# Optimization experiments

Measured on AMD Instinct MI355X. Metric: run time of the kernel, lower is better.

Reference implementation:

```python
import jax, jax.numpy as jnp
import numpy as np
import math

MAX_L = 2          # max spherical-harmonic order
C = 16             # channels per l (num_channels)
LAYERS = 2         # num_CG_layers
CUT = 0.5          # hard_cut_rad


def _cg_single(j1, m1, j2, m2, j, m):
    # Racah formula for Clebsch-Gordan coefficient <j1 m1 j2 m2 | j m>
    if m1 + m2 != m:
        return 0.0
    f = math.factorial
    pre = math.sqrt((2 * j + 1) * f(j + j1 - j2) * f(j - j1 + j2) * f(j1 + j2 - j) / f(j1 + j2 + j + 1))
    pre *= math.sqrt(f(j + m) * f(j - m) * f(j1 - m1) * f(j1 + m1) * f(j2 - m2) * f(j2 + m2))
    s = 0.0
    for k in range(max(0, j2 - j - m1, j1 + m2 - j), min(j1 + j2 - j, j1 - m1, j2 + m2) + 1):
        s += (-1) ** k / (f(k) * f(j1 + j2 - j - k) * f(j1 - m1 - k) * f(j2 + m2 - k) * f(j - j2 + m1 + k) * f(j - j1 - m2 + k))
    return pre * s


PAIRS = {l: [(l1, l2) for l1 in range(MAX_L + 1) for l2 in range(MAX_L + 1) if abs(l1 - l2) <= l <= l1 + l2]
         for l in range(MAX_L + 1)}
CG = {}
for _l in range(MAX_L + 1):
    for (_l1, _l2) in PAIRS[_l]:
        t = np.zeros((2 * _l1 + 1, 2 * _l2 + 1, 2 * _l + 1), np.float32)
        for i1 in range(2 * _l1 + 1):
            for i2 in range(2 * _l2 + 1):
                m = (i1 - _l1) + (i2 - _l2)
                if -_l <= m <= _l:
                    t[i1, i2, m + _l] = _cg_single(_l1, i1 - _l1, _l2, i2 - _l2, _l, m)
        CG[(_l1, _l2, _l)] = jnp.asarray(t)


def _sph(rel_pos):
    # real spherical harmonics Y_l^m of relative positions, l=0..2; [B,N,N,2l+1]
    r = jnp.sqrt(jnp.sum(rel_pos ** 2, -1)) + 1e-6
    x = rel_pos[..., 0] / r
    y = rel_pos[..., 1] / r
    z = rel_pos[..., 2] / r
    Y0 = jnp.full(r.shape + (1,), 0.28209479, rel_pos.dtype)
    Y1 = 0.48860251 * jnp.stack([y, z, x], -1)
    Y2 = jnp.stack([1.09254843 * x * y, 1.09254843 * y * z, 0.31539157 * (3.0 * z * z - 1.0),
                    1.09254843 * x * z, 0.54627422 * (x * x - y * y)], -1)
    return [Y0, Y1, Y2]


def _cgprod(A, B, diag):
    # CG tensor product; full product concatenates outer-product channels (c,d),
    # Diag product pairs channels diagonally (c with c).
    out = []
    for l in range(MAX_L + 1):
        segs = []
        for (l1, l2) in PAIRS[l]:
            cg = CG[(l1, l2, l)]
            if diag:
                segs.append(jnp.einsum('bnmc,bnuc,muk->bnkc', A[l1], B[l2], cg))
            else:
                s = jnp.einsum('bnmc,bnud,muk->bnkcd', A[l1], B[l2], cg)
                segs.append(s.reshape(s.shape[:3] + (-1,)))
        out.append(jnp.concatenate(segs, -1))
    return out


def _normalize(parts):
    # NormalizeVecArr: divide part_l by (2l+1)*||part_l||_F / num_channels
    return [p * (C / ((2 * l + 1) * jnp.linalg.norm(p))) for l, p in enumerate(parts)]


def reference(v0, v1, v2, rel_pos, norms, Wr0, Wr1, Wr2, Wn0, Wn1, Wn2):
    verts = [v0, v1, v2]
    Y = _sph(rel_pos)
    # sphx: sum sph over neighbor axis j (einsum 'bijmc->bimc'), broadcast to C channels
    sphx = []
    for y in Y:
        s = y.sum(2)  # [B,N,2l+1]
        sphx.append(jnp.broadcast_to(s[..., None], s.shape + (C,)))
    conn = (norms < CUT).astype(rel_pos.dtype)  # [B,N,N] connectivity mask
    Wr = [Wr0, Wr1, Wr2]
    Wn = [Wn0, Wn1, Wn2]
    scal = []
    for layer in range(LAYERS):
        cg_rel = _cgprod(verts, sphx, diag=False)
        rel_mixed = [jnp.einsum('bnkp,pc->bnkc', cg_rel[l], Wr[l][layer]) for l in range(MAX_L + 1)]
        # message pass: masked gather-sum over neighbors
        mp = [jnp.einsum('bij,bjkc->bikc', conn, rel_mixed[l]) for l in range(MAX_L + 1)]
        cg_nl = _cgprod(mp, mp, diag=True)
        nl_mixed = [jnp.einsum('bnkp,pc->bnkc', cg_nl[l], Wn[l][layer]) for l in range(MAX_L + 1)]
        verts = _normalize(nl_mixed)
        # GetScalars: l=0 part plus per-l SO(3)-invariant norms sum_m v^2
        s0 = verts[0][:, :, 0, :]                                   # [B,N,C]
        sn = [jnp.sum(verts[l] * verts[l], axis=2) for l in range(MAX_L + 1)]
        scal.append(jnp.concatenate([s0] + sn, -1))                 # [B,N,4C]
    return jnp.concatenate(scal, -1)  # [B,N,LAYERS*4*C]


def setup_inputs():
    B, N = 32, 128
    ks = jax.random.split(jax.random.key(0), 11)
    return {
        'v0': jax.random.normal(ks[0], (B, N, 1, C), jnp.float32),
        'v1': jax.random.normal(ks[1], (B, N, 3, C), jnp.float32),
        'v2': jax.random.normal(ks[2], (B, N, 5, C), jnp.float32),
        'rel_pos': jax.random.normal(ks[3], (B, N, N, 3), jnp.float32),
        'norms': jax.random.uniform(ks[4], (B, N, N), jnp.float32),
        'Wr0': jax.random.normal(ks[5], (LAYERS, 3 * C * C, C), jnp.float32),
        'Wr1': jax.random.normal(ks[6], (LAYERS, 6 * C * C, C), jnp.float32),
        'Wr2': jax.random.normal(ks[7], (LAYERS, 6 * C * C, C), jnp.float32),
        'Wn0': jax.random.normal(ks[8], (LAYERS, 3 * C, C), jnp.float32),
        'Wn1': jax.random.normal(ks[9], (LAYERS, 6 * C, C), jnp.float32),
        'Wn2': jax.random.normal(ks[10], (LAYERS, 6 * C, C), jnp.float32),
    }
```

## Files before the change

kernel.cpp:

```cpp
#include <hip/hip_runtime.h>

#define NN 128

__constant__ int E_l [15] = {0,0,0, 1,1,1,1,1,1, 2,2,2,2,2,2};
__constant__ int E_l1[15] = {0,1,2, 0,1,1,1,2,2, 0,1,1,2,2,2};
__constant__ int E_l2[15] = {0,1,2, 1,0,1,2,1,2, 2,1,2,0,1,2};
__constant__ int E_cg[15] = {0,1,10, 35,44,53,80,125,170, 245,270,315,390,415,490};
__constant__ int E_t [15] = {0,16,32, 48,96,144,192,240,288, 336,416,496,576,656,736};

__device__ __forceinline__ double dfact(int n){
    const double F[9] = {1.0,1.0,2.0,6.0,24.0,120.0,720.0,5040.0,40320.0};
    return F[n];
}

__device__ float cg_single(int j1,int m1,int j2,int m2,int j,int m){
    if (m1 + m2 != m) return 0.0f;
    double pre = sqrt((2.0*j+1.0)*dfact(j+j1-j2)*dfact(j-j1+j2)*dfact(j1+j2-j)/dfact(j1+j2+j+1));
    pre *= sqrt(dfact(j+m)*dfact(j-m)*dfact(j1-m1)*dfact(j1+m1)*dfact(j2-m2)*dfact(j2+m2));
    int k0 = 0;
    if (j2-j-m1 > k0) k0 = j2-j-m1;
    if (j1+m2-j > k0) k0 = j1+m2-j;
    int k1 = j1+j2-j;
    if (j1-m1 < k1) k1 = j1-m1;
    if (j2+m2 < k1) k1 = j2+m2;
    double s = 0.0;
    for (int k = k0; k <= k1; ++k){
        double d = dfact(k)*dfact(j1+j2-j-k)*dfact(j1-m1-k)*dfact(j2+m2-k)*dfact(j-j2+m1+k)*dfact(j-j1-m2+k);
        s += ((k & 1) ? -1.0 : 1.0) / d;
    }
    return (float)(pre * s);
}


__global__ __launch_bounds__(512) void k_setup(const float* __restrict__ Wr0, const float* __restrict__ Wr1,
                                               const float* __restrict__ Wr2,
                                               float* __restrict__ blob, float* __restrict__ wrsum){
    int bx = blockIdx.x, t = threadIdx.x;
    if (bx == 0){
        for (int idx = t; idx < 615; idx += 512){
            int e = 0;
            while (e < 14 && idx >= E_cg[e+1]) e++;
            int l = E_l[e], l1 = E_l1[e], l2 = E_l2[e];
            int local = idx - E_cg[e];
            int dl = 2*l+1, d2 = 2*l2+1;
            int k  = local % dl;
            int r  = local / dl;
            int u  = r % d2;
            int i1 = r / d2;
            blob[idx] = cg_single(l1, i1-l1, l2, u-l2, l, k-l);
        }
        if (t == 0){
            unsigned short* bTB = (unsigned short*)((char*)blob + 2464);
            unsigned char*  bTA = (unsigned char*)((char*)blob + 4096);
            unsigned short* bTC = (unsigned short*)((char*)blob + 4256);
            const int abase[3] = {0,1,4};
            int nt = 0;
            for (int e = 0; e < 15; ++e){
                int l = E_l[e], l1 = E_l1[e], l2 = E_l2[e];
                int dl = 2*l+1, d2 = 2*l2+1;
                for (int k = 0; k < dl; ++k){
                    int st = nt;
                    for (int m = 0; m < 2*l1+1; ++m){
                        int u = k - l + l1 + l2 - m;
                        if (u >= 0 && u <= 2*l2){
                            bTA[nt] = (unsigned char)(((abase[l1]+m)<<4) | (abase[l2]+u));
                            bTC[nt] = (unsigned short)(E_cg[e] + (m*d2+u)*dl + k);
                            nt++;
                        }
                    }
                    int ct = nt - st;
                    for (int c = 0; c < 16; ++c)
                        bTB[E_t[e] + k*16 + c] = (unsigned short)(c | (st<<4) | (ct<<12));
                }
            }
        }
        return;
    }
    int q = (bx-1)*512 + t;
    int layer = q / 3840;
    int r = q % 3840;
    int row = r >> 4, co = r & 15;
    const float* Wr; int pairs; int lrow;
    if (row < 48)       { Wr = Wr0; pairs = 3; lrow = row; }
    else if (row < 144) { Wr = Wr1; pairs = 6; lrow = row - 48; }
    else                { Wr = Wr2; pairs = 6; lrow = row - 144; }
    int pairIdx = lrow >> 4, c = lrow & 15;
    const float* base = Wr + (size_t)layer*pairs*4096 + (size_t)(pairIdx*256 + c*16)*16 + co;
    float s = 0.f;
    #pragma unroll
    for (int d = 0; d < 16; ++d) s += base[d*16];
    wrsum[q] = s;
}

__device__ __forceinline__ void ld_tables(const float* __restrict__ blob, float* CG, unsigned short* TB,
                                          unsigned char* TA, unsigned short* TC, int t){
    for (int i = t; i < 615; i += 512) CG[i] = blob[i];
    const unsigned short* bTB = (const unsigned short*)((const char*)blob + 2464);
    for (int i = t; i < 816; i += 512) TB[i] = bTB[i];
    const unsigned char* bTA = (const unsigned char*)((const char*)blob + 4096);
    if (t < 160) TA[t] = bTA[t];
    const unsigned short* bTC = (const unsigned short*)((const char*)blob + 4256);
    if (t < 160) TC[t] = bTC[t];
}

__device__ __forceinline__ void tfill_full(const float* __restrict__ A, const float* __restrict__ S,
                                           const float* __restrict__ CG, const unsigned short* __restrict__ TB,
                                           const unsigned char* __restrict__ TA, const unsigned short* __restrict__ TC,
                                           float* __restrict__ Tw, int lane){
    #pragma unroll 1
    for (int idx = lane; idx < 816; idx += 64){
        unsigned tbv = TB[idx];
        int c = tbv & 15, st = (tbv>>4) & 255, ct = tbv >> 12;
        float s = 0.f;
        for (int q = 0; q < ct; ++q){
            int ab = TA[st+q];
            s += A[(ab>>4)*16 + c] * S[ab & 15] * CG[TC[st+q]];
        }
        Tw[idx] = s;
    }
}

__device__ __forceinline__ void tfill_diag(const float* __restrict__ M,
                                           const float* __restrict__ CG, const unsigned short* __restrict__ TB,
                                           const unsigned char* __restrict__ TA, const unsigned short* __restrict__ TC,
                                           float* __restrict__ Tw, int lane){
    #pragma unroll 1
    for (int idx = lane; idx < 816; idx += 64){
        unsigned tbv = TB[idx];
        int c = tbv & 15, st = (tbv>>4) & 255, ct = tbv >> 12;
        float s = 0.f;
        for (int q = 0; q < ct; ++q){
            int ab = TA[st+q];
            s += M[(ab>>4)*16 + c] * M[(ab&15)*16 + c] * CG[TC[st+q]];
        }
        Tw[idx] = s;
    }
}

__device__ __forceinline__ float mix_out(const float* __restrict__ WT, const float* __restrict__ Tw, int o){
    int krow = o >> 4, co = o & 15;
    int l = krow == 0 ? 0 : (krow < 4 ? 1 : 2);
    int k = krow - (l==0?0:(l==1?1:4));
    int np = l==0?3:6;
    int tb = l==0?0:(l==1?48:336);
    int rb = l==0?0:(l==1?48:144);
    int dl = 2*l+1;
    float acc = 0.f;
    const float4* Wp = (const float4*)&WT[co*244 + rb];
    #pragma unroll 1
    for (int pq = 0; pq < np; ++pq){
        const float4* Tp = (const float4*)&Tw[tb + (pq*dl + k)*16];
        float4 a0=Tp[0],a1=Tp[1],a2=Tp[2],a3=Tp[3];
        float4 b0=Wp[pq*4],b1=Wp[pq*4+1],b2=Wp[pq*4+2],b3=Wp[pq*4+3];
        acc += a0.x*b0.x+a0.y*b0.y+a0.z*b0.z+a0.w*b0.w
             + a1.x*b1.x+a1.y*b1.y+a1.z*b1.z+a1.w*b1.w
             + a2.x*b2.x+a2.y*b2.y+a2.z*b2.z+a2.w*b2.w
             + a3.x*b3.x+a3.y*b3.y+a3.z*b3.z+a3.w*b3.w;
    }
    return acc;
}

__global__ __launch_bounds__(512) void k_rel0(const float* __restrict__ v0, const float* __restrict__ v1,
                                              const float* __restrict__ v2, const float* __restrict__ rel_pos,
                                              const float* __restrict__ blob, const float* __restrict__ wrsumL,
                                              float* __restrict__ sphx_ws, float* __restrict__ rel){
    __shared__ float CG[616];
    __shared__ unsigned short TB[816];
    __shared__ unsigned char TA[160];
    __shared__ unsigned short TC[160];
    __shared__ float WT[16*244];
    __shared__ float AL[8][144];
    __shared__ float SX[8][12];
    __shared__ __align__(16) float TS[8][816];
    int t = threadIdx.x, w = t >> 6, lane = t & 63;
    int node0 = blockIdx.x * 8, node = node0 + w;
    ld_tables(blob, CG, TB, TA, TC, t);
    #pragma unroll 1
    for (int i = t; i < 3840; i += 512) WT[(i&15)*244 + (i>>4)] = wrsumL[i];
    #pragma unroll 1
    for (int i = t; i < 1152; i += 512){
        int n = i/144, o = i%144, nd = node0+n;
        float v;
        if (o < 16)      v = v0[(size_t)nd*16 + o];
        else if (o < 64) v = v1[(size_t)nd*48 + (o-16)];
        else             v = v2[(size_t)nd*80 + (o-64)];
        AL[n][o] = v;
    }
    {
        const float* rp = rel_pos + (size_t)node * (NN*3);
        float a[9];
        #pragma unroll
        for (int i = 0; i < 9; ++i) a[i] = 0.f;
        #pragma unroll
        for (int rr = 0; rr < 2; ++rr){
            int j = lane + rr*64;
            float x = rp[j*3], y = rp[j*3+1], z = rp[j*3+2];
            float rn = sqrtf(x*x+y*y+z*z) + 1e-6f;
            x /= rn; y /= rn; z /= rn;
            a[0] += 0.28209479f;
            a[1] += 0.48860251f*y; a[2] += 0.48860251f*z; a[3] += 0.48860251f*x;
            a[4] += 1.09254843f*x*y; a[5] += 1.09254843f*y*z;
            a[6] += 0.31539157f*(3.f*z*z-1.f);
            a[7] += 1.09254843f*x*z; a[8] += 0.54627422f*(x*x-y*y);
        }
        #pragma unroll
        for (int i = 0; i < 9; ++i){
            float vv = a[i];
            for (int off = 32; off; off >>= 1) vv += __shfl_down(vv, off, 64);
            if (lane == 0){ SX[w][i] = vv; sphx_ws[(size_t)node*9 + i] = vv; }
        }
    }
    __syncthreads();
    tfill_full(&AL[w][0], &SX[w][0], CG, TB, TA, TC, &TS[w][0], lane);
    __syncthreads();
    float* relw = rel + (size_t)node * 144;
    #pragma unroll 1
    for (int o = lane; o < 144; o += 64) relw[o] = mix_out(WT, &TS[w][0], o);
}

__global__ __launch_bounds__(512) void k_mp(const float* __restrict__ norms, const float* __restrict__ rel,
                                            const float* __restrict__ blob,
                                            const float* __restrict__ Wn0, const float* __restrict__ Wn1,
                                            const float* __restrict__ Wn2, int layer,
                                            float* __restrict__ nl, float* __restrict__ part){
    __shared__ float CG[616];
    __shared__ unsigned short TB[816];
    __shared__ unsigned char TA[160];
    __shared__ unsigned short TC[160];
    __shared__ float WT[16*244];
    __shared__ float C4[8][128];
    __shared__ float MP[8][144];
    __shared__ __align__(16) float TS[8][816];
    __shared__ float RED[24];
    int t = threadIdx.x, w = t >> 6, lane = t & 63;
    int node0 = blockIdx.x * 8, node = node0 + w;
    int b = node0 >> 7;
    ld_tables(blob, CG, TB, TA, TC, t);
    #pragma unroll 1
    for (int i = t; i < 768;  i += 512) WT[(i&15)*244 + (i>>4)]        = Wn0[(size_t)layer*768  + i];
    #pragma unroll 1
    for (int i = t; i < 1536; i += 512) WT[(i&15)*244 + 48  + (i>>4)]  = Wn1[(size_t)layer*1536 + i];
    #pragma unroll 1
    for (int i = t; i < 1536; i += 512) WT[(i&15)*244 + 144 + (i>>4)]  = Wn2[(size_t)layer*1536 + i];
    #pragma unroll 1
    for (int i = t; i < 1024; i += 512){
        int n = i >> 7, j = i & 127;
        C4[n][j] = (norms[(size_t)(node0+n)*NN + j] < 0.5f) ? 1.f : 0.f;
    }
    const float4* r4 = (const float4*)(rel + (size_t)b * NN * 144);
    float4 rA = r4[t];
    float4 rB = r4[512 + t];
    float4 rC = (t < 128) ? r4[1024 + t] : make_float4(0.f,0.f,0.f,0.f);
    float a0 = 0.f, a1 = 0.f, a2 = 0.f;
    float4* s4 = (float4*)&TS[0][0];
    #pragma unroll 1
    for (int r = 0; r < 4; ++r){
        __syncthreads();
        s4[t] = rA; s4[512+t] = rB; if (t < 128) s4[1024+t] = rC;
        __syncthreads();
        if (r < 3){
            rA = r4[(r+1)*1152 + t];
            rB = r4[(r+1)*1152 + 512 + t];
            if (t < 128) rC = r4[(r+1)*1152 + 1024 + t];
        }
        #pragma unroll 4
        for (int jj = 0; jj < 32; ++jj){
            float cn = C4[w][r*32 + jj];
            const float* row = &TS[0][0] + jj*144;
            a0 += cn * row[lane];
            a1 += cn * row[64 + lane];
            if (lane < 16) a2 += cn * row[128 + lane];
        }
    }
    __syncthreads();
    MP[w][lane] = a0; MP[w][64+lane] = a1; if (lane < 16) MP[w][128+lane] = a2;
    __syncthreads();
    tfill_diag(&MP[w][0], CG, TB, TA, TC, &TS[w][0], lane);
    __syncthreads();
    float pz0 = 0.f, pz1 = 0.f, pz2 = 0.f;
    float* nlw = nl + (size_t)node * 144;
    #pragma unroll 1
    for (int o = lane; o < 144; o += 64){
        float acc = mix_out(WT, &TS[w][0], o);
        nlw[o] = acc;
        float sq = acc*acc;
        int krow = o >> 4;
        if (krow == 0) pz0 += sq; else if (krow < 4) pz1 += sq; else pz2 += sq;
    }
    for (int off = 32; off; off >>= 1){
        pz0 += __shfl_down(pz0, off, 64);
        pz1 += __shfl_down(pz1, off, 64);
        pz2 += __shfl_down(pz2, off, 64);
    }
    if (lane == 0){ RED[w] = pz0; RED[8+w] = pz1; RED[16+w] = pz2; }
    __syncthreads();
    if (t < 3){
        float s = 0.f;
        #pragma unroll
        for (int q = 0; q < 8; ++q) s += RED[t*8 + q];
        part[blockIdx.x*4 + t] = s;
    }
}

__global__ __launch_bounds__(512) void k_eb(const float* __restrict__ blob, const float* __restrict__ wrsumL1,
                                            const float* __restrict__ part, const float* __restrict__ nl,
                                            const float* __restrict__ sphx_ws, float* __restrict__ rel,
                                            float* __restrict__ out){
    __shared__ float CG[616];
    __shared__ unsigned short TB[816];
    __shared__ unsigned char TA[160];
    __shared__ unsigned short TC[160];
    __shared__ float WT[16*244];
    __shared__ float AL[8][144];
    __shared__ float SX[8][12];
    __shared__ __align__(16) float TS[8][816];
    __shared__ float RED[24];
    __shared__ float SC[3];
    int t = threadIdx.x, w = t >> 6, lane = t & 63;
    int node0 = blockIdx.x * 8, node = node0 + w;
    ld_tables(blob, CG, TB, TA, TC, t);
    #pragma unroll 1
    for (int i = t; i < 3840; i += 512) WT[(i&15)*244 + (i>>4)] = wrsumL1[i];
    {
        float q0 = part[t*4], q1 = part[t*4+1], q2 = part[t*4+2];
        for (int off = 32; off; off >>= 1){
            q0 += __shfl_down(q0, off, 64);
            q1 += __shfl_down(q1, off, 64);
            q2 += __shfl_down(q2, off, 64);
        }
        if (lane == 0){ RED[w] = q0; RED[8+w] = q1; RED[16+w] = q2; }
    }
    __syncthreads();
    if (t < 3){
        float s = 0.f;
        #pragma unroll
        for (int q = 0; q < 8; ++q) s += RED[t*8 + q];
        SC[t] = 16.f / ((2*t+1) * sqrtf(s));
    }
    __syncthreads();
    float sc0 = SC[0], sc1 = SC[1], sc2 = SC[2];
    #pragma unroll 1
    for (int i = t; i < 1152; i += 512){
        int n = i/144, o = i%144, krow = o >> 4;
        float scl = krow == 0 ? sc0 : (krow < 4 ? sc1 : sc2);
        AL[n][o] = nl[(size_t)(node0+n)*144 + o] * scl;
    }
    if (t < 72) SX[t/9][t%9] = sphx_ws[(size_t)node0*9 + t];
    __syncthreads();
    if (t < 128){
        int n = t >> 4, c = t & 15;
        float s0 = AL[n][c];
        float sn0 = s0*s0, sn1 = 0.f, sn2 = 0.f;
        #pragma unroll
        for (int k = 0; k < 3; ++k){ float v = AL[n][16 + k*16 + c]; sn1 += v*v; }
        #pragma unroll
        for (int k = 0; k < 5; ++k){ float v = AL[n][64 + k*16 + c]; sn2 += v*v; }
        float* ob = out + (size_t)(node0+n)*128;
        ob[c] = s0; ob[16+c] = sn0; ob[32+c] = sn1; ob[48+c] = sn2;
    }
    tfill_full(&AL[w][0], &SX[w][0], CG, TB, TA, TC, &TS[w][0], lane);
    __syncthreads();
    float* relw = rel + (size_t)node * 144;
    #pragma unroll 1
    for (int o = lane; o < 144; o += 64) relw[o] = mix_out(WT, &TS[w][0], o);
}

__global__ __launch_bounds__(512) void k_e2(const float* __restrict__ part, const float* __restrict__ nl,
                                            float* __restrict__ out){
    __shared__ float RED[24];
    __shared__ float SC[3];
    __shared__ float VV[8][144];
    int t = threadIdx.x, w = t >> 6, lane = t & 63;
    int node0 = blockIdx.x * 8;
    {
        float q0 = part[t*4], q1 = part[t*4+1], q2 = part[t*4+2];
        for (int off = 32; off; off >>= 1){
            q0 += __shfl_down(q0, off, 64);
            q1 += __shfl_down(q1, off, 64);
            q2 += __shfl_down(q2, off, 64);
        }
        if (lane == 0){ RED[w] = q0; RED[8+w] = q1; RED[16+w] = q2; }
    }
    __syncthreads();
    if (t < 3){
        float s = 0.f;
        #pragma unroll
        for (int q = 0; q < 8; ++q) s += RED[t*8 + q];
        SC[t] = 16.f / ((2*t+1) * sqrtf(s));
    }
    __syncthreads();
    float sc0 = SC[0], sc1 = SC[1], sc2 = SC[2];
    #pragma unroll 1
    for (int i = t; i < 1152; i += 512){
        int n = i/144, o = i%144, krow = o >> 4;
        float scl = krow == 0 ? sc0 : (krow < 4 ? sc1 : sc2);
        VV[n][o] = nl[(size_t)(node0+n)*144 + o] * scl;
    }
    __syncthreads();
    if (t < 128){
        int n = t >> 4, c = t & 15;
        float s0 = VV[n][c];
        float sn0 = s0*s0, sn1 = 0.f, sn2 = 0.f;
        #pragma unroll
        for (int k = 0; k < 3; ++k){ float v = VV[n][16 + k*16 + c]; sn1 += v*v; }
        #pragma unroll
        for (int k = 0; k < 5; ++k){ float v = VV[n][64 + k*16 + c]; sn2 += v*v; }
        float* ob = out + (size_t)(node0+n)*128 + 64;
        ob[c] = s0; ob[16+c] = sn0; ob[32+c] = sn1; ob[48+c] = sn2;
    }
}

extern "C" void kernel_launch(void* const* d_in, const int* in_sizes, int n_in,
                              void* d_out, int out_size, void* d_ws, size_t ws_size,
                              hipStream_t stream){
    const float* v0      = (const float*)d_in[0];
    const float* v1      = (const float*)d_in[1];
    const float* v2      = (const float*)d_in[2];
    const float* rel_pos = (const float*)d_in[3];
    const float* norms   = (const float*)d_in[4];
    const float* Wr0     = (const float*)d_in[5];
    const float* Wr1     = (const float*)d_in[6];
    const float* Wr2     = (const float*)d_in[7];
    const float* Wn0     = (const float*)d_in[8];
    const float* Wn1     = (const float*)d_in[9];
    const float* Wn2     = (const float*)d_in[10];
    float* out = (float*)d_out;
    float* ws  = (float*)d_ws;

    float* blob  = ws + 0;
    float* wrsum = ws + 1152;
    float* sphx  = ws + 8832;
    float* rel   = ws + 45696;
    float* nl    = ws + 635520;
    float* part  = ws + 1225344;

    k_setup<<<16, 512, 0, stream>>>(Wr0, Wr1, Wr2, blob, wrsum);
    k_rel0 <<<512, 512, 0, stream>>>(v0, v1, v2, rel_pos, blob, wrsum, sphx, rel);
    k_mp   <<<512, 512, 0, stream>>>(norms, rel, blob, Wn0, Wn1, Wn2, 0, nl, part);
    k_eb   <<<512, 512, 0, stream>>>(blob, wrsum + 3840, part, nl, sphx, rel, out);
    k_mp   <<<512, 512, 0, stream>>>(norms, rel, blob, Wn0, Wn1, Wn2, 1, nl, part);
    k_e2   <<<512, 512, 0, stream>>>(part, nl, out);
}
```

Baseline: 203.3 us.

## Fuse all stages into one persistent kernel with global barriers

Six kernel launches are merged into a single persistent kernel of 256 blocks, each handling 16 nodes, with atomic-counter grid barriers between stages. CG tables are computed per block in shared memory instead of staged through a global blob, and per-node intermediates stay in shared memory rather than round-tripping through workspace. This targets launch overhead and global traffic, but halves the block count, serializes two nodes per wave, and relies on all 256 blocks being co-resident for the spin barrier.

```diff
diff --git a/kernel.cpp b/kernel.cpp
--- a/kernel.cpp
+++ b/kernel.cpp
@@ -31,78 +31,6 @@
     return (float)(pre * s);
 }
 
-
-__global__ __launch_bounds__(512) void k_setup(const float* __restrict__ Wr0, const float* __restrict__ Wr1,
-                                               const float* __restrict__ Wr2,
-                                               float* __restrict__ blob, float* __restrict__ wrsum){
-    int bx = blockIdx.x, t = threadIdx.x;
-    if (bx == 0){
-        for (int idx = t; idx < 615; idx += 512){
-            int e = 0;
-            while (e < 14 && idx >= E_cg[e+1]) e++;
-            int l = E_l[e], l1 = E_l1[e], l2 = E_l2[e];
-            int local = idx - E_cg[e];
-            int dl = 2*l+1, d2 = 2*l2+1;
-            int k  = local % dl;
-            int r  = local / dl;
-            int u  = r % d2;
-            int i1 = r / d2;
-            blob[idx] = cg_single(l1, i1-l1, l2, u-l2, l, k-l);
-        }
-        if (t == 0){
-            unsigned short* bTB = (unsigned short*)((char*)blob + 2464);
-            unsigned char*  bTA = (unsigned char*)((char*)blob + 4096);
-            unsigned short* bTC = (unsigned short*)((char*)blob + 4256);
-            const int abase[3] = {0,1,4};
-            int nt = 0;
-            for (int e = 0; e < 15; ++e){
-                int l = E_l[e], l1 = E_l1[e], l2 = E_l2[e];
-                int dl = 2*l+1, d2 = 2*l2+1;
-                for (int k = 0; k < dl; ++k){
-                    int st = nt;
-                    for (int m = 0; m < 2*l1+1; ++m){
-                        int u = k - l + l1 + l2 - m;
-                        if (u >= 0 && u <= 2*l2){
-                            bTA[nt] = (unsigned char)(((abase[l1]+m)<<4) | (abase[l2]+u));
-                            bTC[nt] = (unsigned short)(E_cg[e] + (m*d2+u)*dl + k);
-                            nt++;
-                        }
-                    }
-                    int ct = nt - st;
-                    for (int c = 0; c < 16; ++c)
-                        bTB[E_t[e] + k*16 + c] = (unsigned short)(c | (st<<4) | (ct<<12));
-                }
-            }
-        }
-        return;
-    }
-    int q = (bx-1)*512 + t;
-    int layer = q / 3840;
-    int r = q % 3840;
-    int row = r >> 4, co = r & 15;
-    const float* Wr; int pairs; int lrow;
-    if (row < 48)       { Wr = Wr0; pairs = 3; lrow = row; }
-    else if (row < 144) { Wr = Wr1; pairs = 6; lrow = row - 48; }
-    else                { Wr = Wr2; pairs = 6; lrow = row - 144; }
-    int pairIdx = lrow >> 4, c = lrow & 15;
-    const float* base = Wr + (size_t)layer*pairs*4096 + (size_t)(pairIdx*256 + c*16)*16 + co;
-    float s = 0.f;
-    #pragma unroll
-    for (int d = 0; d < 16; ++d) s += base[d*16];
-    wrsum[q] = s;
-}
-
-__device__ __forceinline__ void ld_tables(const float* __restrict__ blob, float* CG, unsigned short* TB,
-                                          unsigned char* TA, unsigned short* TC, int t){
-    for (int i = t; i < 615; i += 512) CG[i] = blob[i];
-    const unsigned short* bTB = (const unsigned short*)((const char*)blob + 2464);
-    for (int i = t; i < 816; i += 512) TB[i] = bTB[i];
-    const unsigned char* bTA = (const unsigned char*)((const char*)blob + 4096);
-    if (t < 160) TA[t] = bTA[t];
-    const unsigned short* bTC = (const unsigned short*)((const char*)blob + 4256);
-    if (t < 160) TC[t] = bTC[t];
-}
-
 __device__ __forceinline__ void tfill_full(const float* __restrict__ A, const float* __restrict__ S,
                                            const float* __restrict__ CG, const unsigned short* __restrict__ TB,
                                            const unsigned char* __restrict__ TA, const unsigned short* __restrict__ TC,
@@ -160,34 +88,119 @@
     return acc;
 }
 
-__global__ __launch_bounds__(512) void k_rel0(const float* __restrict__ v0, const float* __restrict__ v1,
-                                              const float* __restrict__ v2, const float* __restrict__ rel_pos,
-                                              const float* __restrict__ blob, const float* __restrict__ wrsumL,
-                                              float* __restrict__ sphx_ws, float* __restrict__ rel){
+__device__ __forceinline__ void gbar(int* bar, int inst){
+    __syncthreads();
+    if (threadIdx.x == 0){
+        __threadfence();
+        int* cnt = bar + inst*16;
+        int* flg = bar + inst*16 + 8;
+        int a = __hip_atomic_fetch_add(cnt, 1, __ATOMIC_ACQ_REL, __HIP_MEMORY_SCOPE_AGENT);
+        if (a == 255)
+            __hip_atomic_store(flg, 1, __ATOMIC_RELEASE, __HIP_MEMORY_SCOPE_AGENT);
+        long spins = 0;
+        while (__hip_atomic_load(flg, __ATOMIC_ACQUIRE, __HIP_MEMORY_SCOPE_AGENT) == 0){
+            __builtin_amdgcn_s_sleep(2);
+            if (++spins > 200000000L) break;
+        }
+        __threadfence();
+    }
+    __syncthreads();
+}
+
+__global__ __launch_bounds__(512) void k_all(
+    const float* __restrict__ v0, const float* __restrict__ v1, const float* __restrict__ v2,
+    const float* __restrict__ rel_pos, const float* __restrict__ norms,
+    const float* __restrict__ Wr0, const float* __restrict__ Wr1, const float* __restrict__ Wr2,
+    const float* __restrict__ Wn0, const float* __restrict__ Wn1, const float* __restrict__ Wn2,
+    float* __restrict__ out,
+    float* __restrict__ wrsum_ws, float* __restrict__ rel,
+    float* __restrict__ part0, float* __restrict__ part1, int* __restrict__ bar)
+{
     __shared__ float CG[616];
     __shared__ unsigned short TB[816];
     __shared__ unsigned char TA[160];
     __shared__ unsigned short TC[160];
-    __shared__ float WT[16*244];
-    __shared__ float AL[8][144];
-    __shared__ float SX[8][12];
+    __shared__ float WT[3904];
+    __shared__ float AL[16][144];
+    __shared__ float SX[16][12];
+    __shared__ unsigned char CN[16][128];
     __shared__ __align__(16) float TS[8][816];
-    int t = threadIdx.x, w = t >> 6, lane = t & 63;
-    int node0 = blockIdx.x * 8, node = node0 + w;
-    ld_tables(blob, CG, TB, TA, TC, t);
-    #pragma unroll 1
-    for (int i = t; i < 3840; i += 512) WT[(i&15)*244 + (i>>4)] = wrsumL[i];
-    #pragma unroll 1
-    for (int i = t; i < 1152; i += 512){
-        int n = i/144, o = i%144, nd = node0+n;
-        float v;
-        if (o < 16)      v = v0[(size_t)nd*16 + o];
-        else if (o < 64) v = v1[(size_t)nd*48 + (o-16)];
-        else             v = v2[(size_t)nd*80 + (o-64)];
-        AL[n][o] = v;
-    }
-    {
-        const float* rp = rel_pos + (size_t)node * (NN*3);
+    __shared__ float RED[24];
+    __shared__ float SCL[4];
+
+    const int t = threadIdx.x, w = t >> 6, lane = t & 63;
+    const int bid = blockIdx.x;
+    const int node0 = bid * 16;
+    const int batch = bid >> 3;
+    const int n0 = w*2, n1 = w*2 + 1;
+
+    #pragma unroll 1
+    for (int idx = t; idx < 615; idx += 512){
+        int e = 0;
+        while (e < 14 && idx >= E_cg[e+1]) e++;
+        int l = E_l[e], l1 = E_l1[e], l2 = E_l2[e];
+        int local = idx - E_cg[e];
+        int dl = 2*l+1, d2 = 2*l2+1;
+        int k  = local % dl;
+        int r  = local / dl;
+        int u  = r % d2;
+        int i1 = r / d2;
+        CG[idx] = cg_single(l1, i1-l1, l2, u-l2, l, k-l);
+    }
+    if (t < 51){
+        int p = t, e = 0, k = 0;
+        for (e = 0; e < 15; ++e){
+            int dl = 2*E_l[e]+1;
+            if (p < dl){ k = p; break; }
+            p -= dl;
+        }
+        int st = 0; bool stop = false;
+        for (int pe = 0; pe < 15 && !stop; ++pe){
+            int l = E_l[pe], l1 = E_l1[pe], l2 = E_l2[pe], dl = 2*l+1;
+            for (int kk = 0; kk < dl; ++kk){
+                if (pe == e && kk == k){ stop = true; break; }
+                int u0 = kk - l + l1 + l2;
+                int lo = u0 - 2*l2; if (lo < 0) lo = 0;
+                int hi = u0; if (hi > 2*l1) hi = 2*l1;
+                if (hi >= lo) st += hi - lo + 1;
+            }
+        }
+        int l = E_l[e], l1 = E_l1[e], l2 = E_l2[e], dl = 2*l+1, d2 = 2*l2+1;
+        int ab = (l1==0?0:(l1==1?1:4)), sb = (l2==0?0:(l2==1?1:4));
+        int u0 = k - l + l1 + l2;
+        int lo = u0 - 2*l2; if (lo < 0) lo = 0;
+        int hi = u0; if (hi > 2*l1) hi = 2*l1;
+        int ct = (hi >= lo) ? (hi - lo + 1) : 0;
+        int nt = st;
+        for (int m = lo; m <= hi; ++m){
+            int u = u0 - m;
+            TA[nt] = (unsigned char)(((ab+m)<<4) | (sb+u));
+            TC[nt] = (unsigned short)(E_cg[e] + (m*d2+u)*dl + k);
+            nt++;
+        }
+        for (int c = 0; c < 16; ++c)
+            TB[E_t[e] + k*16 + c] = (unsigned short)(c | (st<<4) | (ct<<12));
+    }
+    if (bid < 15){
+        int q = bid*512 + t;
+        int layer = q / 3840;
+        int r = q % 3840;
+        int row = r >> 4, co = r & 15;
+        const float* Wr; int pairs; int lrow;
+        if (row < 48)       { Wr = Wr0; pairs = 3; lrow = row; }
+        else if (row < 144) { Wr = Wr1; pairs = 6; lrow = row - 48; }
+        else                { Wr = Wr2; pairs = 6; lrow = row - 144; }
+        int pairIdx = lrow >> 4, c = lrow & 15;
+        const float* base = Wr + (size_t)layer*pairs*4096 + (size_t)(pairIdx*256 + c*16)*16 + co;
+        float s = 0.f;
+        #pragma unroll
+        for (int d = 0; d < 16; ++d) s += base[d*16];
+        wrsum_ws[q] = s;
+    }
+    #pragma unroll 1
+    for (int nn = 0; nn < 2; ++nn){
+        int n = w*2 + nn, gn = node0 + n;
+        const float* rp = rel_pos + (size_t)gn * (NN*3);
         float a[9];
         #pragma unroll
         for (int i = 0; i < 9; ++i) a[i] = 0.f;
@@ -207,206 +220,152 @@
         for (int i = 0; i < 9; ++i){
             float vv = a[i];
             for (int off = 32; off; off >>= 1) vv += __shfl_down(vv, off, 64);
-            if (lane == 0){ SX[w][i] = vv; sphx_ws[(size_t)node*9 + i] = vv; }
-        }
-    }
+            if (lane == 0) SX[n][i] = vv;
+        }
+    }
+    #pragma unroll 1
+    for (int i = t; i < 2304; i += 512){
+        int n = i/144, o = i%144, gn = node0+n;
+        float v;
+        if (o < 16)      v = v0[(size_t)gn*16 + o];
+        else if (o < 64) v = v1[(size_t)gn*48 + (o-16)];
+        else             v = v2[(size_t)gn*80 + (o-64)];
+        AL[n][o] = v;
+    }
+    #pragma unroll 1
+    for (int i = t; i < 2048; i += 512){
+        int n = i >> 7, j = i & 127;
+        CN[n][j] = (norms[(size_t)(node0+n)*NN + j] < 0.5f) ? 1 : 0;
+    }
+    gbar(bar, 0);
+
+    #pragma unroll 1
+    for (int i = t; i < 3840; i += 512) WT[(i&15)*244 + (i>>4)] = wrsum_ws[i];
     __syncthreads();
-    tfill_full(&AL[w][0], &SX[w][0], CG, TB, TA, TC, &TS[w][0], lane);
-    __syncthreads();
-    float* relw = rel + (size_t)node * 144;
-    #pragma unroll 1
-    for (int o = lane; o < 144; o += 64) relw[o] = mix_out(WT, &TS[w][0], o);
-}
-
-__global__ __launch_bounds__(512) void k_mp(const float* __restrict__ norms, const float* __restrict__ rel,
-                                            const float* __restrict__ blob,
-                                            const float* __restrict__ Wn0, const float* __restrict__ Wn1,
-                                            const float* __restrict__ Wn2, int layer,
-                                            float* __restrict__ nl, float* __restrict__ part){
-    __shared__ float CG[616];
-    __shared__ unsigned short TB[816];
-    __shared__ unsigned char TA[160];
-    __shared__ unsigned short TC[160];
-    __shared__ float WT[16*244];
-    __shared__ float C4[8][128];
-    __shared__ float MP[8][144];
-    __shared__ __align__(16) float TS[8][816];
-    __shared__ float RED[24];
-    int t = threadIdx.x, w = t >> 6, lane = t & 63;
-    int node0 = blockIdx.x * 8, node = node0 + w;
-    int b = node0 >> 7;
-    ld_tables(blob, CG, TB, TA, TC, t);
-    #pragma unroll 1
-    for (int i = t; i < 768;  i += 512) WT[(i&15)*244 + (i>>4)]        = Wn0[(size_t)layer*768  + i];
-    #pragma unroll 1
-    for (int i = t; i < 1536; i += 512) WT[(i&15)*244 + 48  + (i>>4)]  = Wn1[(size_t)layer*1536 + i];
-    #pragma unroll 1
-    for (int i = t; i < 1536; i += 512) WT[(i&15)*244 + 144 + (i>>4)]  = Wn2[(size_t)layer*1536 + i];
-    #pragma unroll 1
-    for (int i = t; i < 1024; i += 512){
-        int n = i >> 7, j = i & 127;
-        C4[n][j] = (norms[(size_t)(node0+n)*NN + j] < 0.5f) ? 1.f : 0.f;
-    }
-    const float4* r4 = (const float4*)(rel + (size_t)b * NN * 144);
-    float4 rA = r4[t];
-    float4 rB = r4[512 + t];
-    float4 rC = (t < 128) ? r4[1024 + t] : make_float4(0.f,0.f,0.f,0.f);
-    float a0 = 0.f, a1 = 0.f, a2 = 0.f;
-    float4* s4 = (float4*)&TS[0][0];
-    #pragma unroll 1
-    for (int r = 0; r < 4; ++r){
-        __syncthreads();
-        s4[t] = rA; s4[512+t] = rB; if (t < 128) s4[1024+t] = rC;
-        __syncthreads();
-        if (r < 3){
-            rA = r4[(r+1)*1152 + t];
-            rB = r4[(r+1)*1152 + 512 + t];
-            if (t < 128) rC = r4[(r+1)*1152 + 1024 + t];
-        }
-        #pragma unroll 4
-        for (int jj = 0; jj < 32; ++jj){
-            float cn = C4[w][r*32 + jj];
-            const float* row = &TS[0][0] + jj*144;
-            a0 += cn * row[lane];
-            a1 += cn * row[64 + lane];
-            if (lane < 16) a2 += cn * row[128 + lane];
-        }
-    }
-    __syncthreads();
-    MP[w][lane] = a0; MP[w][64+lane] = a1; if (lane < 16) MP[w][128+lane] = a2;
-    __syncthreads();
-    tfill_diag(&MP[w][0], CG, TB, TA, TC, &TS[w][0], lane);
-    __syncthreads();
-    float pz0 = 0.f, pz1 = 0.f, pz2 = 0.f;
-    float* nlw = nl + (size_t)node * 144;
-    #pragma unroll 1
-    for (int o = lane; o < 144; o += 64){
-        float acc = mix_out(WT, &TS[w][0], o);
-        nlw[o] = acc;
-        float sq = acc*acc;
-        int krow = o >> 4;
-        if (krow == 0) pz0 += sq; else if (krow < 4) pz1 += sq; else pz2 += sq;
-    }
-    for (int off = 32; off; off >>= 1){
-        pz0 += __shfl_down(pz0, off, 64);
-        pz1 += __shfl_down(pz1, off, 64);
-        pz2 += __shfl_down(pz2, off, 64);
-    }
-    if (lane == 0){ RED[w] = pz0; RED[8+w] = pz1; RED[16+w] = pz2; }
-    __syncthreads();
-    if (t < 3){
-        float s = 0.f;
-        #pragma unroll
-        for (int q = 0; q < 8; ++q) s += RED[t*8 + q];
-        part[blockIdx.x*4 + t] = s;
-    }
-}
-
-__global__ __launch_bounds__(512) void k_eb(const float* __restrict__ blob, const float* __restrict__ wrsumL1,
-                                            const float* __restrict__ part, const float* __restrict__ nl,
-                                            const float* __restrict__ sphx_ws, float* __restrict__ rel,
-                                            float* __restrict__ out){
-    __shared__ float CG[616];
-    __shared__ unsigned short TB[816];
-    __shared__ unsigned char TA[160];
-    __shared__ unsigned short TC[160];
-    __shared__ float WT[16*244];
-    __shared__ float AL[8][144];
-    __shared__ float SX[8][12];
-    __shared__ __align__(16) float TS[8][816];
-    __shared__ float RED[24];
-    __shared__ float SC[3];
-    int t = threadIdx.x, w = t >> 6, lane = t & 63;
-    int node0 = blockIdx.x * 8, node = node0 + w;
-    ld_tables(blob, CG, TB, TA, TC, t);
-    #pragma unroll 1
-    for (int i = t; i < 3840; i += 512) WT[(i&15)*244 + (i>>4)] = wrsumL1[i];
-    {
-        float q0 = part[t*4], q1 = part[t*4+1], q2 = part[t*4+2];
+    #pragma unroll 1
+    for (int nn = 0; nn < 2; ++nn){
+        int n = w*2 + nn, gn = node0 + n;
+        tfill_full(&AL[n][0], &SX[n][0], CG, TB, TA, TC, &TS[w][0], lane);
+        __syncthreads();
+        float* relw = rel + (size_t)gn * 144;
+        #pragma unroll 1
+        for (int o = lane; o < 144; o += 64) relw[o] = mix_out(WT, &TS[w][0], o);
+        __syncthreads();
+    }
+    gbar(bar, 1);
+
+    #pragma unroll 1
+    for (int layer = 0; layer < 2; ++layer){
+        float* part = layer == 0 ? part0 : part1;
+        #pragma unroll 1
+        for (int i = t; i < 768;  i += 512) WT[(i&15)*244 + (i>>4)]       = Wn0[(size_t)layer*768  + i];
+        #pragma unroll 1
+        for (int i = t; i < 1536; i += 512) WT[(i&15)*244 + 48  + (i>>4)] = Wn1[(size_t)layer*1536 + i];
+        #pragma unroll 1
+        for (int i = t; i < 1536; i += 512) WT[(i&15)*244 + 144 + (i>>4)] = Wn2[(size_t)layer*1536 + i];
+        {
+            const float4* r4 = (const float4*)(rel + (size_t)batch * (NN*144));
+            float a00=0.f,a01=0.f,a02=0.f, a10=0.f,a11=0.f,a12=0.f;
+            float4* s4 = (float4*)&TS[0][0];
+            #pragma unroll 1
+            for (int r = 0; r < 4; ++r){
+                __syncthreads();
+                #pragma unroll 1
+                for (int i = t; i < 1152; i += 512) s4[i] = r4[r*1152 + i];
+                __syncthreads();
+                #pragma unroll 4
+                for (int jj = 0; jj < 32; ++jj){
+                    float c0 = (float)CN[n0][r*32 + jj];
+                    float c1 = (float)CN[n1][r*32 + jj];
+                    const float* row = &TS[0][0] + jj*144;
+                    float x0 = row[lane], x1 = row[64 + lane];
+                    a00 += c0*x0; a01 += c0*x1;
+                    a10 += c1*x0; a11 += c1*x1;
+                    if (lane < 16){
+                        float x2 = row[128 + lane];
+                        a02 += c0*x2; a12 += c1*x2;
+                    }
+                }
+            }
+            __syncthreads();
+            AL[n0][lane] = a00; AL[n0][64+lane] = a01; if (lane < 16) AL[n0][128+lane] = a02;
+            AL[n1][lane] = a10; AL[n1][64+lane] = a11; if (lane < 16) AL[n1][128+lane] = a12;
+            __syncthreads();
+        }
+        float pz0 = 0.f, pz1 = 0.f, pz2 = 0.f;
+        #pragma unroll 1
+        for (int nn = 0; nn < 2; ++nn){
+            int n = w*2 + nn;
+            tfill_diag(&AL[n][0], CG, TB, TA, TC, &TS[w][0], lane);
+            __syncthreads();
+            #pragma unroll 1
+            for (int o = lane; o < 144; o += 64){
+                float acc = mix_out(WT, &TS[w][0], o);
+                AL[n][o] = acc;
+                float sq = acc*acc;
+                int krow = o >> 4;
+                if (krow == 0) pz0 += sq; else if (krow < 4) pz1 += sq; else pz2 += sq;
+            }
+            __syncthreads();
+        }
         for (int off = 32; off; off >>= 1){
-            q0 += __shfl_down(q0, off, 64);
-            q1 += __shfl_down(q1, off, 64);
-            q2 += __shfl_down(q2, off, 64);
-        }
-        if (lane == 0){ RED[w] = q0; RED[8+w] = q1; RED[16+w] = q2; }
-    }
-    __syncthreads();
-    if (t < 3){
-        float s = 0.f;
-        #pragma unroll
-        for (int q = 0; q < 8; ++q) s += RED[t*8 + q];
-        SC[t] = 16.f / ((2*t+1) * sqrtf(s));
-    }
-    __syncthreads();
-    float sc0 = SC[0], sc1 = SC[1], sc2 = SC[2];
-    #pragma unroll 1
-    for (int i = t; i < 1152; i += 512){
-        int n = i/144, o = i%144, krow = o >> 4;
-        float scl = krow == 0 ? sc0 : (krow < 4 ? sc1 : sc2);
-        AL[n][o] = nl[(size_t)(node0+n)*144 + o] * scl;
-    }
-    if (t < 72) SX[t/9][t%9] = sphx_ws[(size_t)node0*9 + t];
-    __syncthreads();
-    if (t < 128){
-        int n = t >> 4, c = t & 15;
-        float s0 = AL[n][c];
-        float sn0 = s0*s0, sn1 = 0.f, sn2 = 0.f;
-        #pragma unroll
-        for (int k = 0; k < 3; ++k){ float v = AL[n][16 + k*16 + c]; sn1 += v*v; }
-        #pragma unroll
-        for (int k = 0; k < 5; ++k){ float v = AL[n][64 + k*16 + c]; sn2 += v*v; }
-        float* ob = out + (size_t)(node0+n)*128;
-        ob[c] = s0; ob[16+c] = sn0; ob[32+c] = sn1; ob[48+c] = sn2;
-    }
-    tfill_full(&AL[w][0], &SX[w][0], CG, TB, TA, TC, &TS[w][0], lane);
-    __syncthreads();
-    float* relw = rel + (size_t)node * 144;
-    #pragma unroll 1
-    for (int o = lane; o < 144; o += 64) relw[o] = mix_out(WT, &TS[w][0], o);
-}
-
-__global__ __launch_bounds__(512) void k_e2(const float* __restrict__ part, const float* __restrict__ nl,
-                                            float* __restrict__ out){
-    __shared__ float RED[24];
-    __shared__ float SC[3];
-    __shared__ float VV[8][144];
-    int t = threadIdx.x, w = t >> 6, lane = t & 63;
-    int node0 = blockIdx.x * 8;
-    {
-        float q0 = part[t*4], q1 = part[t*4+1], q2 = part[t*4+2];
-        for (int off = 32; off; off >>= 1){
-            q0 += __shfl_down(q0, off, 64);
-            q1 += __shfl_down(q1, off, 64);
-            q2 += __shfl_down(q2, off, 64);
-        }
-        if (lane == 0){ RED[w] = q0; RED[8+w] = q1; RED[16+w] = q2; }
-    }
-    __syncthreads();
-    if (t < 3){
-        float s = 0.f;
-        #pragma unroll
-        for (int q = 0; q < 8; ++q) s += RED[t*8 + q];
-        SC[t] = 16.f / ((2*t+1) * sqrtf(s));
-    }
-    __syncthreads();
-    float sc0 = SC[0], sc1 = SC[1], sc2 = SC[2];
-    #pragma unroll 1
-    for (int i = t; i < 1152; i += 512){
-        int n = i/144, o = i%144, krow = o >> 4;
-        float scl = krow == 0 ? sc0 : (krow < 4 ? sc1 : sc2);
-        VV[n][o] = nl[(size_t)(node0+n)*144 + o] * scl;
-    }
-    __syncthreads();
-    if (t < 128){
-        int n = t >> 4, c = t & 15;
-        float s0 = VV[n][c];
-        float sn0 = s0*s0, sn1 = 0.f, sn2 = 0.f;
-        #pragma unroll
-        for (int k = 0; k < 3; ++k){ float v = VV[n][16 + k*16 + c]; sn1 += v*v; }
-        #pragma unroll
-        for (int k = 0; k < 5; ++k){ float v = VV[n][64 + k*16 + c]; sn2 += v*v; }
-        float* ob = out + (size_t)(node0+n)*128 + 64;
-        ob[c] = s0; ob[16+c] = sn0; ob[32+c] = sn1; ob[48+c] = sn2;
+            pz0 += __shfl_down(pz0, off, 64);
+            pz1 += __shfl_down(pz1, off, 64);
+            pz2 += __shfl_down(pz2, off, 64);
+        }
+        if (lane == 0){ RED[w] = pz0; RED[8+w] = pz1; RED[16+w] = pz2; }
+        __syncthreads();
+        if (t < 3){
+            float s = 0.f;
+            #pragma unroll
+            for (int q = 0; q < 8; ++q) s += RED[t*8 + q];
+            part[bid*3 + t] = s;
+        }
+        gbar(bar, 2 + layer*2);
+
+        if (t < 4) SCL[t] = 0.f;
+        __syncthreads();
+        #pragma unroll 1
+        for (int i = t; i < 768; i += 512) atomicAdd(&SCL[i % 3], part[i]);
+        __syncthreads();
+        if (t < 3) SCL[t] = 16.f / ((2*t+1) * sqrtf(SCL[t]));
+        __syncthreads();
+        {
+            float s0 = SCL[0], s1 = SCL[1], s2 = SCL[2];
+            #pragma unroll 1
+            for (int i = t; i < 2304; i += 512){
+                int n = i/144, o = i%144, krow = o >> 4;
+                AL[n][o] *= (krow == 0 ? s0 : (krow < 4 ? s1 : s2));
+            }
+        }
+        __syncthreads();
+        if (t < 256){
+            int n = t >> 4, c = t & 15;
+            float s0 = AL[n][c];
+            float sn0 = s0*s0, sn1 = 0.f, sn2 = 0.f;
+            #pragma unroll
+            for (int k = 0; k < 3; ++k){ float v = AL[n][16 + k*16 + c]; sn1 += v*v; }
+            #pragma unroll
+            for (int k = 0; k < 5; ++k){ float v = AL[n][64 + k*16 + c]; sn2 += v*v; }
+            float* ob = out + (size_t)(node0+n)*128 + layer*64;
+            ob[c] = s0; ob[16+c] = sn0; ob[32+c] = sn1; ob[48+c] = sn2;
+        }
+        if (layer == 0){
+            #pragma unroll 1
+            for (int i = t; i < 3840; i += 512) WT[(i&15)*244 + (i>>4)] = wrsum_ws[3840 + i];
+            __syncthreads();
+            #pragma unroll 1
+            for (int nn = 0; nn < 2; ++nn){
+                int n = w*2 + nn, gn = node0 + n;
+                tfill_full(&AL[n][0], &SX[n][0], CG, TB, TA, TC, &TS[w][0], lane);
+                __syncthreads();
+                float* relw = rel + (size_t)gn * 144;
+                #pragma unroll 1
+                for (int o = lane; o < 144; o += 64) relw[o] = mix_out(WT, &TS[w][0], o);
+                __syncthreads();
+            }
+            gbar(bar, 3);
+        }
     }
 }
 
@@ -427,17 +386,14 @@
     float* out = (float*)d_out;
     float* ws  = (float*)d_ws;
 
-    float* blob  = ws + 0;
-    float* wrsum = ws + 1152;
-    float* sphx  = ws + 8832;
-    float* rel   = ws + 45696;
-    float* nl    = ws + 635520;
-    float* part  = ws + 1225344;
-
-    k_setup<<<16, 512, 0, stream>>>(Wr0, Wr1, Wr2, blob, wrsum);
-    k_rel0 <<<512, 512, 0, stream>>>(v0, v1, v2, rel_pos, blob, wrsum, sphx, rel);
-    k_mp   <<<512, 512, 0, stream>>>(norms, rel, blob, Wn0, Wn1, Wn2, 0, nl, part);
-    k_eb   <<<512, 512, 0, stream>>>(blob, wrsum + 3840, part, nl, sphx, rel, out);
-    k_mp   <<<512, 512, 0, stream>>>(norms, rel, blob, Wn0, Wn1, Wn2, 1, nl, part);
-    k_e2   <<<512, 512, 0, stream>>>(part, nl, out);
-}
+    float* wrsum = ws + 0;
+    float* rel   = ws + 7680;
+    float* part0 = ws + 597504;
+    float* part1 = ws + 598272;
+    int*   bar   = (int*)(ws + 599040);
+
+    hipMemsetAsync(bar, 0, 80*sizeof(int), stream);
+    k_all<<<256, 512, 0, stream>>>(v0, v1, v2, rel_pos, norms,
+                                   Wr0, Wr1, Wr2, Wn0, Wn1, Wn2,
+                                   out, wrsum, rel, part0, part1, bar);
+}
```

After: 311.2 us. 1.53x slower.
